# Performance work log

Hardware: AMD Instinct MI355X
Metric: run time of the kernel (lower is better)

Reference implementation:

```python
import jax, jax.numpy as jnp
import numpy as np


def setup_inputs() -> dict:
    key = jax.random.key(0)
    T, B, N = 2048, 16, 2048
    spikes = (jax.random.uniform(key, (T, B, N)) < 0.05).astype(jnp.float32)
    return {"input_spikes": spikes, "duration": 100}


def reference(input_spikes, duration):
    # Causal sliding-window (boxcar) sum over the time axis of length `duration`,
    # equivalent to conv1d with a ones kernel and causal padding, then clamp to [0,1].
    # psp[t] = clip( sum_{k=max(0,t-duration+1)}^{t} x[k], 0, 1 )
    T = input_spikes.shape[0]
    c = jnp.cumsum(input_spikes, axis=0)                     # [T, ...]
    pad = [(duration, 0)] + [(0, 0)] * (input_spikes.ndim - 1)
    c_shift = jnp.pad(c, pad)[:T]                            # c[t-duration], 0 for t<duration
    win = c - c_shift
    return jnp.clip(win, 0.0, 1.0)
```

## Files before the change

kernel.cpp:

```cpp
#include <hip/hip_runtime.h>


#define T_TOTAL 2048
#define M_COLS  (16 * 2048)
#define M4      (M_COLS / 4)
#define TW      (T_TOTAL / 32)

__global__ __launch_bounds__(256) void pack_bits(
    const float4* __restrict__ x,
    uint4* __restrict__ bm)
{
    const int c4  = blockIdx.x * 256 + threadIdx.x;
    const int twb = blockIdx.y;

    unsigned w0 = 0, w1 = 0, w2 = 0, w3 = 0;
    const float4* xp = x + (size_t)(twb * 32) * M4 + c4;
    #pragma unroll
    for (int i = 0; i < 32; ++i) {
        float4 v = xp[(size_t)i * M4];
        w0 |= (v.x != 0.0f ? 1u : 0u) << i;
        w1 |= (v.y != 0.0f ? 1u : 0u) << i;
        w2 |= (v.z != 0.0f ? 1u : 0u) << i;
        w3 |= (v.w != 0.0f ? 1u : 0u) << i;
    }
    bm[(size_t)twb * M4 + c4] = make_uint4(w0, w1, w2, w3);
}

#define TB 8

__global__ __launch_bounds__(256) void window_or(
    const uint4* __restrict__ bm,
    const int*  __restrict__ dur_p,
    float4* __restrict__ out)
{
    const int c4 = blockIdx.x * 256 + threadIdx.x;
    const int t0 = blockIdx.y * TB;
    const int duration = dur_p[0];

    #pragma unroll
    for (int k = 0; k < TB; ++k) {
        const int t = t0 + k;
        int L = t - (duration - 1);
        if (L < 0) L = 0;
        const int tw = t >> 5, r  = t & 31;
        const int Lw = L >> 5, Lr = L & 31;

        unsigned ax = 0, ay = 0, az = 0, aw = 0;
        for (int wi = Lw; wi <= tw; ++wi) {
            unsigned m = 0xffffffffu;
            if (wi == tw) m &= (2u << r) - 1u;
            if (wi == Lw) m &= ~((1u << Lr) - 1u);
            uint4 w = bm[(size_t)wi * M4 + c4];
            ax |= w.x & m; ay |= w.y & m; az |= w.z & m; aw |= w.w & m;
        }
        float4 o;
        o.x = ax ? 1.0f : 0.0f;
        o.y = ay ? 1.0f : 0.0f;
        o.z = az ? 1.0f : 0.0f;
        o.w = aw ? 1.0f : 0.0f;
        out[(size_t)t * M4 + c4] = o;
    }
}

extern "C" void kernel_launch(void* const* d_in, const int* in_sizes, int n_in,
                              void* d_out, int out_size, void* d_ws, size_t ws_size,
                              hipStream_t stream) {
    const float4* x     = (const float4*)d_in[0];
    const int*    dur_p = (const int*)d_in[1];
    float4*       out   = (float4*)d_out;
    uint4*        bm    = (uint4*)d_ws;

    pack_bits<<<dim3(M4 / 256, TW), 256, 0, stream>>>(x, bm);
    window_or<<<dim3(M4 / 256, T_TOTAL / TB), 256, 0, stream>>>(bm, dur_p, out);
}
```

Baseline: 464.6 us.

## Use persistent grid-stride window kernel with unrolled loads and nontemporal stores

```diff
diff --git a/kernel.cpp b/kernel.cpp
--- a/kernel.cpp
+++ b/kernel.cpp
@@ -5,6 +5,8 @@
 #define M_COLS  (16 * 2048)
 #define M4      (M_COLS / 4)
 #define TW      (T_TOTAL / 32)
+
+typedef float f32x4 __attribute__((ext_vector_type(4)));
 
 __global__ __launch_bounds__(256) void pack_bits(
     const float4* __restrict__ x,
@@ -26,39 +28,58 @@
     bm[(size_t)twb * M4 + c4] = make_uint4(w0, w1, w2, w3);
 }
 
-#define TB 8
+#define K2_GRID 1024
+#define NCHUNK  (T_TOTAL * (M4 / 256))
 
-__global__ __launch_bounds__(256) void window_or(
+__global__ __launch_bounds__(256) void window_or_lin(
     const uint4* __restrict__ bm,
     const int*  __restrict__ dur_p,
-    float4* __restrict__ out)
+    float* __restrict__ out)
 {
-    const int c4 = blockIdx.x * 256 + threadIdx.x;
-    const int t0 = blockIdx.y * TB;
     const int duration = dur_p[0];
+    const int tid = threadIdx.x;
 
-    #pragma unroll
-    for (int k = 0; k < TB; ++k) {
-        const int t = t0 + k;
-        int L = t - (duration - 1);
-        if (L < 0) L = 0;
+    for (int ci = blockIdx.x; ci < NCHUNK; ci += K2_GRID) {
+        const int t  = ci >> 5;
+        const int c4 = ((ci & 31) << 8) + tid;
+        int L = t - (duration - 1); if (L < 0) L = 0;
         const int tw = t >> 5, r  = t & 31;
         const int Lw = L >> 5, Lr = L & 31;
 
         unsigned ax = 0, ay = 0, az = 0, aw = 0;
-        for (int wi = Lw; wi <= tw; ++wi) {
-            unsigned m = 0xffffffffu;
-            if (wi == tw) m &= (2u << r) - 1u;
-            if (wi == Lw) m &= ~((1u << Lr) - 1u);
-            uint4 w = bm[(size_t)wi * M4 + c4];
-            ax |= w.x & m; ay |= w.y & m; az |= w.z & m; aw |= w.w & m;
+        if (tw - Lw <= 4) {
+            uint4 w[5];
+            #pragma unroll
+            for (int j = 0; j < 5; ++j) {
+                int wi = Lw + j; if (wi > TW - 1) wi = TW - 1;
+                w[j] = bm[(size_t)wi * M4 + c4];
+            }
+            #pragma unroll
+            for (int j = 0; j < 5; ++j) {
+                const int wi = Lw + j;
+                unsigned m = (wi > tw) ? 0u : 0xffffffffu;
+                if (wi == tw) m &= (2u << r) - 1u;
+                if (wi == Lw) m &= ~((1u << Lr) - 1u);
+                ax |= w[j].x & m; ay |= w[j].y & m;
+                az |= w[j].z & m; aw |= w[j].w & m;
+            }
+        } else {
+            for (int wi = Lw; wi <= tw; ++wi) {
+                unsigned m = 0xffffffffu;
+                if (wi == tw) m &= (2u << r) - 1u;
+                if (wi == Lw) m &= ~((1u << Lr) - 1u);
+                uint4 w = bm[(size_t)wi * M4 + c4];
+                ax |= w.x & m; ay |= w.y & m; az |= w.z & m; aw |= w.w & m;
+            }
         }
-        float4 o;
+
+        f32x4 o;
         o.x = ax ? 1.0f : 0.0f;
         o.y = ay ? 1.0f : 0.0f;
         o.z = az ? 1.0f : 0.0f;
         o.w = aw ? 1.0f : 0.0f;
-        out[(size_t)t * M4 + c4] = o;
+        __builtin_nontemporal_store(
+            o, (f32x4*)(out + ((size_t)ci * 1024 + (size_t)tid * 4)));
     }
 }
 
@@ -67,9 +88,9 @@
                               hipStream_t stream) {
     const float4* x     = (const float4*)d_in[0];
     const int*    dur_p = (const int*)d_in[1];
-    float4*       out   = (float4*)d_out;
+    float*        out   = (float*)d_out;
     uint4*        bm    = (uint4*)d_ws;
 
     pack_bits<<<dim3(M4 / 256, TW), 256, 0, stream>>>(x, bm);
-    window_or<<<dim3(M4 / 256, T_TOTAL / TB), 256, 0, stream>>>(bm, dur_p, out);
+    window_or_lin<<<K2_GRID, 256, 0, stream>>>(bm, dur_p, out);
 }
```

Measured after the change: 461.0 us. Within noise of the previous version (-0.8%).
